# Kernel optimization log

Measured on AMD Instinct MI355X. Metric: run time of the kernel, lower is better.

The kernel has to match this reference:

```python
import jax, jax.numpy as jnp
import numpy as np

B, L, HEADS, D_HEAD = 2, 2048, 16, 64
D_MODEL = HEADS * D_HEAD            # 1024
D_BI = D_MODEL * 4 // 2             # 2048 (bilinear GLU width)
D_PROJ = D_MODEL * 3 + 2 * D_BI
DEPTH = 0                           # block depth < 2 -> token shift active
NEG_INF = -1e10


def _ln(x, g, b, eps=1e-5):
    m = jnp.mean(x, axis=-1, keepdims=True)
    v = jnp.var(x, axis=-1, keepdims=True)
    return (x - m) * jax.lax.rsqrt(v + eps) * g + b


def _shift(x, n):
    # F.pad(x, (0,0,n,-n)): shift along seq dim by n, zero-fill at front
    return jnp.pad(x, ((0, 0), (n, 0), (0, 0)))[:, : x.shape[1], :]


def setup_inputs() -> dict:
    key = jax.random.key(0)
    ks = jax.random.split(key, 3)
    x = jax.random.normal(ks[0], (B, L, D_MODEL), jnp.float32)
    w_in = jax.random.normal(ks[1], (D_MODEL, D_PROJ), jnp.float32) * (D_MODEL ** -0.5)
    # note: torch init zeros out_proj; we use small random weights so backward is non-trivial
    w_out = jax.random.normal(ks[2], (D_MODEL + D_BI, D_MODEL), jnp.float32) * 0.02
    slopes = jnp.concatenate([2.0 ** jnp.linspace(0.0, -6.0, HEADS // 2),
                              jnp.zeros(HEADS - HEADS // 2)]).astype(jnp.float32)
    return {
        "x": x,
        "in_ln_g": jnp.ones(D_MODEL, jnp.float32), "in_ln_b": jnp.zeros(D_MODEL, jnp.float32),
        "mid_ln_g": jnp.ones(D_PROJ, jnp.float32), "mid_ln_b": jnp.zeros(D_PROJ, jnp.float32),
        "out_ln_g": jnp.ones(D_MODEL, jnp.float32), "out_ln_b": jnp.zeros(D_MODEL, jnp.float32),
        "w_in": w_in, "w_out": w_out, "slopes": slopes,
    }


def reference(x, in_ln_g, in_ln_b, mid_ln_g, mid_ln_b, out_ln_g, out_ln_b, w_in, w_out, slopes):
    b, l, d = x.shape
    x = _ln(x, in_ln_g, in_ln_b)
    if DEPTH < 2:
        x = jnp.concatenate([
            _shift(x[..., : d // 4], 1),
            x[..., d // 4: d - d // 8],
            _shift(x[..., d - d // 8:], 2),
        ], axis=-1)
    h = _ln(x @ w_in, mid_ln_g, mid_ln_b)
    q, k, v, p1, p2 = jnp.split(h, [D_MODEL, 2 * D_MODEL, 3 * D_MODEL, 3 * D_MODEL + D_BI], axis=-1)
    to_heads = lambda t: t.reshape(b, l, HEADS, D_HEAD).transpose(0, 2, 1, 3)  # b h l d
    q, k, v = to_heads(q), to_heads(k), to_heads(v)
    logits = jnp.einsum('bhid,bhjd->bhij', q, k) * (D_HEAD ** -0.5)
    pos = jnp.arange(l)
    alibi = pos[None, None, None, :].astype(logits.dtype) * slopes[None, :, None, None]
    causal = jnp.where(pos[:, None] >= pos[None, :], 0.0, NEG_INF).astype(logits.dtype)
    a = jax.nn.softmax(logits + alibi + causal, axis=-1)
    o = jnp.einsum('bhij,bhjd->bhid', a, v).transpose(0, 2, 1, 3).reshape(b, l, d)
    return _ln(jnp.concatenate([o, p1 * p2], axis=-1) @ w_out, out_ln_g, out_ln_b)
```

## Files before the change

### kernel.cpp

```cpp
#include <hip/hip_runtime.h>

#define B_ 2
#define L_ 2048
#define HEADS_ 16
#define DH_ 64
#define DM_ 1024
#define DBI_ 2048
#define DPROJ_ 7168
#define NTOK (B_*L_)
#define DCAT (DM_ + DBI_)

typedef __bf16 bf16;
typedef __attribute__((ext_vector_type(8))) __bf16 bf16x8;
typedef __attribute__((ext_vector_type(4))) float floatx4;

typedef __attribute__((address_space(1))) const void gptr_t;
typedef __attribute__((address_space(3))) void lptr_t;

__device__ __forceinline__ void g2l16(const void* g, void* l) {
    __builtin_amdgcn_global_load_lds((gptr_t*)g, (lptr_t*)l, 16, 0, 0);
}

__global__ __launch_bounds__(256) void transpose_both(const float* __restrict__ w_in,
                                                      const float* __restrict__ w_out,
                                                      bf16* __restrict__ w_inT,
                                                      bf16* __restrict__ w_outT) {
    __shared__ float tile[32][33];
    int l = blockIdx.x;
    const float* in; bf16* outp; int R, C, bx, by;
    if (l < 7168) { in = w_in;  outp = w_inT;  R = DM_;  C = DPROJ_; bx = l % 224; by = l / 224; }
    else { l -= 7168; in = w_out; outp = w_outT; R = DCAT; C = DM_;   bx = l % 32;  by = l / 32; }
    int c0 = bx * 32, r0 = by * 32;
    int x = threadIdx.x & 31, y = threadIdx.x >> 5;
    for (int i = 0; i < 32; i += 8)
        tile[y + i][x] = in[(size_t)(r0 + y + i) * C + (c0 + x)];
    __syncthreads();
    for (int i = 0; i < 32; i += 8)
        outp[(size_t)(c0 + y + i) * R + (r0 + x)] = (bf16)tile[x][y + i];
}

__global__ __launch_bounds__(256) void ln_shift(const float* __restrict__ x,
                                                const float* __restrict__ g,
                                                const float* __restrict__ bb,
                                                bf16* __restrict__ xs) {
    int tok = blockIdx.x;
    int b = tok / L_, l = tok % L_;
    const float* row = x + (size_t)tok * DM_;
    float vals[4];
    float s = 0.f, s2 = 0.f;
    for (int i = 0; i < 4; i++) {
        float v = row[threadIdx.x + i * 256];
        vals[i] = v; s += v; s2 += v * v;
    }
    __shared__ float red[2][4];
    for (int o = 32; o; o >>= 1) { s += __shfl_xor(s, o); s2 += __shfl_xor(s2, o); }
    int w = threadIdx.x >> 6;
    if ((threadIdx.x & 63) == 0) { red[0][w] = s; red[1][w] = s2; }
    __syncthreads();
    s  = red[0][0] + red[0][1] + red[0][2] + red[0][3];
    s2 = red[1][0] + red[1][1] + red[1][2] + red[1][3];
    float mean = s * (1.f / DM_);
    float var  = s2 * (1.f / DM_) - mean * mean;
    float rstd = rsqrtf(var + 1e-5f);
    for (int i = 0; i < 4; i++) {
        int c = threadIdx.x + i * 256;
        float y = (vals[i] - mean) * rstd * g[c] + bb[c];
        int shift = (c < 256) ? 1 : ((c >= 896) ? 2 : 0);
        int dl = l + shift;
        if (dl < L_) xs[((size_t)b * L_ + dl) * DM_ + c] = (bf16)y;
        if (l == 0 && shift) {
            xs[((size_t)b * L_ + 0) * DM_ + c] = (bf16)0.f;
            if (shift == 2) xs[((size_t)b * L_ + 1) * DM_ + c] = (bf16)0.f;
        }
    }
}

__global__ __launch_bounds__(256, 2) void gemm1_k(const bf16* __restrict__ A,
                                                  const bf16* __restrict__ Bt,
                                                  bf16* __restrict__ C) {
    const int K = DM_, N = DPROJ_;
    int lin = blockIdx.x;
    int chunk = lin >> 7, within = lin & 127;
    int m0 = (within >> 3) * 256;
    int n0 = (chunk * 8 + (within & 7)) * 128;
    __shared__ bf16 As[2][256 * 32];
    __shared__ bf16 Bs[2][128 * 32];
    int t = threadIdx.x, lane = t & 63, wave = t >> 6;
    int c = lane & 15, quad = lane >> 4;
    int wm = wave * 64;
    auto stage = [&](int k0, int bsel) {
        #pragma unroll
        for (int s = 0; s < 4; s++) {
            int f = s * 256 + t;
            int row = f >> 2, kp = (f & 3) * 8;
            g2l16(A + (size_t)(m0 + row) * K + k0 + kp, &As[bsel][f * 8]);
        }
        #pragma unroll
        for (int s = 0; s < 2; s++) {
            int f = s * 256 + t;
            int row = f >> 2, kp = (f & 3) * 8;
            g2l16(Bt + (size_t)(n0 + row) * K + k0 + kp, &Bs[bsel][f * 8]);
        }
    };
    floatx4 acc[4][8] = {};
    stage(0, 0);
    int buf = 0;
    for (int k0 = 0; k0 < K; k0 += 32) {
        __syncthreads();
        if (k0 + 32 < K) stage(k0 + 32, buf ^ 1);
        bf16x8 af[4], bfr[8];
        #pragma unroll
        for (int i = 0; i < 4; i++)
            af[i] = *(const bf16x8*)&As[buf][(wm + i * 16 + c) * 32 + quad * 8];
        #pragma unroll
        for (int j = 0; j < 8; j++)
            bfr[j] = *(const bf16x8*)&Bs[buf][(j * 16 + c) * 32 + quad * 8];
        #pragma unroll
        for (int i = 0; i < 4; i++)
            #pragma unroll
            for (int j = 0; j < 8; j++)
                acc[i][j] = __builtin_amdgcn_mfma_f32_16x16x32_bf16(af[i], bfr[j], acc[i][j], 0, 0, 0);
        buf ^= 1;
    }
    #pragma unroll
    for (int i = 0; i < 4; i++)
        #pragma unroll
        for (int j = 0; j < 8; j++)
            #pragma unroll
            for (int r = 0; r < 4; r++) {
                int row = m0 + wm + i * 16 + quad * 4 + r;
                int col = n0 + j * 16 + c;
                C[(size_t)row * N + col] = (bf16)acc[i][j][r];
            }
}

__global__ __launch_bounds__(256) void gemm2_sk(const bf16* __restrict__ A,
                                                const bf16* __restrict__ Bt,
                                                float* __restrict__ P) {
    const int ldA = DCAT, N = DM_;
    int m0 = blockIdx.x * 128, n0 = blockIdx.y * 128, kz = blockIdx.z;
    const bf16* Ak = A + kz * 1024;
    const bf16* Btk = Bt + kz * 1024;
    float* C = P + (size_t)kz * NTOK * DM_;
    __shared__ bf16 As[2][128 * 32];
    __shared__ bf16 Bs[2][128 * 32];
    int t = threadIdx.x, lane = t & 63, wave = t >> 6;
    int c = lane & 15, quad = lane >> 4;
    int wm = (wave >> 1) * 64, wn = (wave & 1) * 64;
    auto stage = [&](int k0, int bsel) {
        #pragma unroll
        for (int s = 0; s < 2; s++) {
            int f = s * 256 + t;
            int row = f >> 2, kp = (f & 3) * 8;
            g2l16(Ak + (size_t)(m0 + row) * ldA + k0 + kp, &As[bsel][f * 8]);
            g2l16(Btk + (size_t)(n0 + row) * ldA + k0 + kp, &Bs[bsel][f * 8]);
        }
    };
    floatx4 acc[4][4] = {};
    stage(0, 0);
    int buf = 0;
    for (int k0 = 0; k0 < 1024; k0 += 32) {
        __syncthreads();
        if (k0 + 32 < 1024) stage(k0 + 32, buf ^ 1);
        bf16x8 af[4], bfr[4];
        #pragma unroll
        for (int i = 0; i < 4; i++)
            af[i] = *(const bf16x8*)&As[buf][(wm + i * 16 + c) * 32 + quad * 8];
        #pragma unroll
        for (int j = 0; j < 4; j++)
            bfr[j] = *(const bf16x8*)&Bs[buf][(wn + j * 16 + c) * 32 + quad * 8];
        #pragma unroll
        for (int i = 0; i < 4; i++)
            #pragma unroll
            for (int j = 0; j < 4; j++)
                acc[i][j] = __builtin_amdgcn_mfma_f32_16x16x32_bf16(af[i], bfr[j], acc[i][j], 0, 0, 0);
        buf ^= 1;
    }
    #pragma unroll
    for (int i = 0; i < 4; i++)
        #pragma unroll
        for (int j = 0; j < 4; j++)
            #pragma unroll
            for (int r = 0; r < 4; r++) {
                int row = m0 + wm + i * 16 + quad * 4 + r;
                int col = n0 + wn + j * 16 + c;
                C[(size_t)row * N + col] = acc[i][j][r];
            }
}

__global__ __launch_bounds__(256) void mid_ln_fused(const bf16* __restrict__ h,
                                                    const float* __restrict__ g,
                                                    const float* __restrict__ bb,
                                                    bf16* __restrict__ Qp,
                                                    bf16* __restrict__ Kp,
                                                    bf16* __restrict__ Vn,
                                                    bf16* __restrict__ A2) {
    int tok = blockIdx.x;
    int b = tok >> 11, l = tok & 2047;
    size_t base = (size_t)tok * DPROJ_;
    int t = threadIdx.x;
    float v[28];
    float s = 0.f, s2 = 0.f;
    for (int i = 0; i < 28; i++) {
        v[i] = (float)h[base + t + i * 256];
        s += v[i]; s2 += v[i] * v[i];
    }
    __shared__ float red[2][4];
    for (int o = 32; o; o >>= 1) { s += __shfl_xor(s, o); s2 += __shfl_xor(s2, o); }
    int w = t >> 6;
    if ((t & 63) == 0) { red[0][w] = s; red[1][w] = s2; }
    __syncthreads();
    s  = red[0][0] + red[0][1] + red[0][2] + red[0][3];
    s2 = red[1][0] + red[1][1] + red[1][2] + red[1][3];
    float mean = s * (1.f / DPROJ_);
    float var  = s2 * (1.f / DPROJ_) - mean * mean;
    float rstd = rsqrtf(var + 1e-5f);
    #pragma unroll
    for (int i = 0; i < 28; i++) {
        int c = t + i * 256;
        v[i] = (v[i] - mean) * rstd * g[c] + bb[c];
    }
    #pragma unroll
    for (int i = 0; i < 12; i++) {
        int c = t + i * 256;
        int sec = c >> 10;
        int cc = c & 1023;
        int hh = cc >> 6, d = cc & 63;
        size_t idx = (((size_t)b * HEADS_ + hh) * L_ + l) * DH_ + d;
        bf16* dst = (sec == 0) ? Qp : (sec == 1) ? Kp : Vn;
        dst[idx] = (bf16)v[i];
    }
    #pragma unroll
    for (int i = 12; i < 20; i++) {
        int c = t + i * 256;
        A2[(size_t)tok * DCAT + DM_ + (c - 3 * DM_)] = (bf16)(v[i] * v[i + 8]);
    }
}

__global__ __launch_bounds__(256) void vt_pack(const bf16* __restrict__ Vn,
                                               bf16* __restrict__ Vt) {
    __shared__ bf16 tile[32][33];
    int bh = blockIdx.z;
    const bf16* in = Vn + (size_t)bh * L_ * DH_;
    bf16* out = Vt + (size_t)bh * DH_ * L_;
    int l0 = blockIdx.x * 32, d0 = blockIdx.y * 32;
    int x = threadIdx.x & 31, y = threadIdx.x >> 5;
    for (int i = 0; i < 32; i += 8)
        tile[y + i][x] = in[(size_t)(l0 + y + i) * DH_ + d0 + x];
    __syncthreads();
    for (int i = 0; i < 32; i += 8)
        out[(size_t)(d0 + y + i) * L_ + l0 + x] = tile[x][y + i];
}

__global__ __launch_bounds__(256, 4) void attn4(const bf16* __restrict__ Qp,
                                                const bf16* __restrict__ Kp,
                                                const bf16* __restrict__ Vt,
                                                const float* __restrict__ slopes,
                                                bf16* __restrict__ A2) {
    int hd = blockIdx.y, b = blockIdx.z;
    int lin = blockIdx.x + 32 * blockIdx.y + 512 * blockIdx.z;
    int xr = blockIdx.x;
    int qt = ((lin >> 8) & 1) ? (31 - xr) : xr;
    int q0 = qt * 64;
    int t = threadIdx.x, lane = t & 63, wave = t >> 6;
    int quad = lane >> 4, c = lane & 15;
    __shared__ bf16 Ks[2 * 64 * 32];
    __shared__ bf16 Vs[2 * 64 * 32];
    __shared__ bf16 Ps[4][16 * 72];
    int bh = b * HEADS_ + hd;
    const bf16* Qb = Qp + (size_t)bh * L_ * DH_;
    const bf16* Kb = Kp + (size_t)bh * L_ * DH_;
    const bf16* Vb = Vt + (size_t)bh * DH_ * L_;
    const float LOG2E = 1.44269504f;
    float slopeL2 = slopes[hd] * LOG2E;
    const float qscale = 0.125f * LOG2E;

    bf16x8 qf[2];
    int qrow = q0 + wave * 16 + c;
    qf[0] = *(const bf16x8*)(Qb + (size_t)qrow * DH_ + quad * 8);
    qf[1] = *(const bf16x8*)(Qb + (size_t)qrow * DH_ + 32 + quad * 8);
    floatx4 accO[4] = {};
    float lsum[4];
    float mrow[4];
    int i_row0 = q0 + wave * 16 + quad * 4;
    #pragma unroll
    for (int r = 0; r < 4; r++) {
        lsum[r] = 0.f;
        mrow[r] = slopeL2 * (float)(i_row0 + r) + 20.0f;
    }

    int row = t >> 2, kp = (t & 3) * 8;
    bf16* pw = &Ps[wave][0];
    bf16* pwr = pw + (quad * 4) * 72 + c;
    for (int j0 = 0; j0 <= q0; j0 += 64) {
        #pragma unroll
        for (int s = 0; s < 2; s++) {
            g2l16(Kb + (size_t)(j0 + row) * DH_ + s * 32 + kp, &Ks[(s * 256 + t) * 8]);
            g2l16(Vb + (size_t)row * L_ + j0 + s * 32 + kp, &Vs[(s * 256 + t) * 8]);
        }
        __syncthreads();

        bool diag = (j0 == q0);
        #pragma unroll
        for (int nt = 0; nt < 4; nt++) {
            floatx4 sacc = {};
            bf16x8 kf0 = *(const bf16x8*)&Ks[(nt * 16 + c) * 32 + quad * 8];
            bf16x8 kf1 = *(const bf16x8*)&Ks[2048 + (nt * 16 + c) * 32 + quad * 8];
            sacc = __builtin_amdgcn_mfma_f32_16x16x32_bf16(qf[0], kf0, sacc, 0, 0, 0);
            sacc = __builtin_amdgcn_mfma_f32_16x16x32_bf16(qf[1], kf1, sacc, 0, 0, 0);
            int j = j0 + nt * 16 + c;
            float aj = slopeL2 * (float)j;
            #pragma unroll
            for (int r = 0; r < 4; r++) {
                float p = exp2f(fmaf(sacc[r], qscale, aj) - mrow[r]);
                if (diag) p = (j <= i_row0 + r) ? p : 0.f;
                lsum[r] += p;
                pwr[r * 72 + nt * 16] = (bf16)p;
            }
        }
        bf16x8 pf0 = *(const bf16x8*)&pw[c * 72 + quad * 8];
        bf16x8 pf1 = *(const bf16x8*)&pw[c * 72 + 32 + quad * 8];
        #pragma unroll
        for (int nt = 0; nt < 4; nt++) {
            bf16x8 vf0 = *(const bf16x8*)&Vs[(nt * 16 + c) * 32 + quad * 8];
            bf16x8 vf1 = *(const bf16x8*)&Vs[2048 + (nt * 16 + c) * 32 + quad * 8];
            accO[nt] = __builtin_amdgcn_mfma_f32_16x16x32_bf16(pf0, vf0, accO[nt], 0, 0, 0);
            accO[nt] = __builtin_amdgcn_mfma_f32_16x16x32_bf16(pf1, vf1, accO[nt], 0, 0, 0);
        }
        __syncthreads();
    }
    #pragma unroll
    for (int r = 0; r < 4; r++) {
        float l = lsum[r];
        l += __shfl_xor(l, 1);
        l += __shfl_xor(l, 2);
        l += __shfl_xor(l, 4);
        l += __shfl_xor(l, 8);
        lsum[r] = 1.f / l;
    }
    #pragma unroll
    for (int r = 0; r < 4; r++) {
        size_t orow = (size_t)b * L_ + q0 + wave * 16 + quad * 4 + r;
        #pragma unroll
        for (int nt = 0; nt < 4; nt++)
            A2[orow * DCAT + hd * DH_ + nt * 16 + c] = (bf16)(accO[nt][r] * lsum[r]);
    }
}

__global__ __launch_bounds__(256) void out_ln3(const float* __restrict__ P,
                                               const float* __restrict__ g,
                                               const float* __restrict__ bb,
                                               float* __restrict__ out) {
    size_t base = (size_t)blockIdx.x * DM_;
    const size_t stride = (size_t)NTOK * DM_;
    float v[4];
    float s = 0.f, s2 = 0.f;
    for (int i = 0; i < 4; i++) {
        size_t idx = base + threadIdx.x + i * 256;
        v[i] = P[idx] + P[idx + stride] + P[idx + 2 * stride];
        s += v[i]; s2 += v[i] * v[i];
    }
    __shared__ float red[2][4];
    for (int o = 32; o; o >>= 1) { s += __shfl_xor(s, o); s2 += __shfl_xor(s2, o); }
    int w = threadIdx.x >> 6;
    if ((threadIdx.x & 63) == 0) { red[0][w] = s; red[1][w] = s2; }
    __syncthreads();
    s  = red[0][0] + red[0][1] + red[0][2] + red[0][3];
    s2 = red[1][0] + red[1][1] + red[1][2] + red[1][3];
    float mean = s * (1.f / DM_);
    float var  = s2 * (1.f / DM_) - mean * mean;
    float rstd = rsqrtf(var + 1e-5f);
    for (int i = 0; i < 4; i++) {
        int c = threadIdx.x + i * 256;
        out[base + c] = (v[i] - mean) * rstd * g[c] + bb[c];
    }
}

extern "C" void kernel_launch(void* const* d_in, const int* in_sizes, int n_in,
                              void* d_out, int out_size, void* d_ws, size_t ws_size,
                              hipStream_t stream) {
    const float* x     = (const float*)d_in[0];
    const float* in_g  = (const float*)d_in[1];
    const float* in_b  = (const float*)d_in[2];
    const float* mid_g = (const float*)d_in[3];
    const float* mid_b = (const float*)d_in[4];
    const float* out_g = (const float*)d_in[5];
    const float* out_b = (const float*)d_in[6];
    const float* w_in  = (const float*)d_in[7];
    const float* w_out = (const float*)d_in[8];
    const float* slopes = (const float*)d_in[9];
    float* out = (float*)d_out;

    char* ws = (char*)d_ws;
    size_t off = 0;
    auto alloc = [&](size_t n) { char* p = ws + off; off += (n + 255) & ~(size_t)255; return p; };
    bf16* w_inT  = (bf16*)alloc((size_t)DPROJ_ * DM_ * 2);
    bf16* w_outT = (bf16*)alloc((size_t)DM_ * DCAT * 2);
    bf16* xs     = (bf16*)alloc((size_t)NTOK * DM_ * 2);
    bf16* h      = (bf16*)alloc((size_t)NTOK * DPROJ_ * 2);
    bf16* A2     = (bf16*)alloc((size_t)NTOK * DCAT * 2);
    bf16* Qp     = (bf16*)alloc((size_t)NTOK * DM_ * 2);
    bf16* Kp     = (bf16*)alloc((size_t)NTOK * DM_ * 2);
    bf16* Vn     = (bf16*)alloc((size_t)NTOK * DM_ * 2);
    bf16* Vt = xs;
    float* P = (float*)h;

    hipLaunchKernelGGL(transpose_both, dim3(7168 + 3072), dim3(256), 0, stream,
                       w_in, w_out, w_inT, w_outT);
    hipLaunchKernelGGL(ln_shift, dim3(NTOK), dim3(256), 0, stream, x, in_g, in_b, xs);
    hipLaunchKernelGGL(gemm1_k, dim3(896), dim3(256), 0, stream, xs, w_inT, h);
    hipLaunchKernelGGL(mid_ln_fused, dim3(NTOK), dim3(256), 0, stream, h, mid_g, mid_b,
                       Qp, Kp, Vn, A2);
    hipLaunchKernelGGL(vt_pack, dim3(L_ / 32, DH_ / 32, B_ * HEADS_), dim3(256), 0, stream, Vn, Vt);
    hipLaunchKernelGGL(attn4, dim3(32, HEADS_, B_), dim3(256), 0, stream, Qp, Kp, Vt, slopes, A2);
    hipLaunchKernelGGL(gemm2_sk, dim3(NTOK / 128, DM_ / 128, 3), dim3(256), 0, stream,
                       A2, w_outT, P);
    hipLaunchKernelGGL(out_ln3, dim3(NTOK), dim3(256), 0, stream, P, out_g, out_b, out);
}
```

Measured before the change: 320.4 us.

## Rewrite input-projection GEMM with 256x256 tiles, 8 waves, and swizzled LDS pipeline

The first GEMM moves from 256x128 tiles with 4 waves and K-step 32 to 256x256 tiles with 8 waves and K-step 64. It adds an XOR-swizzled LDS layout to avoid bank conflicts and an XCD-aware block-to-tile mapping. It also adds an interleaved schedule that issues the next tile's global-to-LDS loads between MFMA phases, using explicit barriers, waitcnts and setprio. The aim is more data reuse per LDS load and more hidden memory latency. The cost is 128 KB of LDS per block, which likely limits occupancy to one block per CU, plus fragile hand-tuned synchronisation.

```diff
diff --git a/kernel.cpp b/kernel.cpp
--- a/kernel.cpp
+++ b/kernel.cpp
@@ -75,61 +75,109 @@
     }
 }
 
-__global__ __launch_bounds__(256, 2) void gemm1_k(const bf16* __restrict__ A,
-                                                  const bf16* __restrict__ Bt,
-                                                  bf16* __restrict__ C) {
+__global__ __launch_bounds__(512, 2) void gemm1_8p(const bf16* __restrict__ A,
+                                                   const bf16* __restrict__ Bt,
+                                                   bf16* __restrict__ C) {
     const int K = DM_, N = DPROJ_;
     int lin = blockIdx.x;
-    int chunk = lin >> 7, within = lin & 127;
-    int m0 = (within >> 3) * 256;
-    int n0 = (chunk * 8 + (within & 7)) * 128;
-    __shared__ bf16 As[2][256 * 32];
-    __shared__ bf16 Bs[2][128 * 32];
-    int t = threadIdx.x, lane = t & 63, wave = t >> 6;
+    int xcd = lin & 7, idx = lin >> 3;
+    int mt = (xcd >> 2) * 8 + idx / 7;
+    int nt = (xcd & 3) * 7 + idx % 7;
+    int m0 = mt * 256, n0 = nt * 256;
+
+    __shared__ bf16 As[2][256 * 64];
+    __shared__ bf16 Bs[2][256 * 64];
+
+    int t = threadIdx.x;
+    int lane = t & 63;
     int c = lane & 15, quad = lane >> 4;
-    int wm = wave * 64;
-    auto stage = [&](int k0, int bsel) {
-        #pragma unroll
-        for (int s = 0; s < 4; s++) {
-            int f = s * 256 + t;
-            int row = f >> 2, kp = (f & 3) * 8;
-            g2l16(A + (size_t)(m0 + row) * K + k0 + kp, &As[bsel][f * 8]);
-        }
+    int wave = t >> 6;
+    int wm = (wave >> 2) * 128;
+    int wn = (wave & 3) * 64;
+
+    auto stageA = [&](int k0, int bsel, int h) {
         #pragma unroll
         for (int s = 0; s < 2; s++) {
-            int f = s * 256 + t;
-            int row = f >> 2, kp = (f & 3) * 8;
-            g2l16(Bt + (size_t)(n0 + row) * K + k0 + kp, &Bs[bsel][f * 8]);
+            int g = h * 1024 + s * 512 + t;
+            int row = g >> 3;
+            int kc = (g & 7) ^ (row & 7);
+            g2l16(A + (size_t)(m0 + row) * K + (k0 + kc * 8), &As[bsel][g * 8]);
         }
     };
-    floatx4 acc[4][8] = {};
-    stage(0, 0);
-    int buf = 0;
-    for (int k0 = 0; k0 < K; k0 += 32) {
-        __syncthreads();
-        if (k0 + 32 < K) stage(k0 + 32, buf ^ 1);
-        bf16x8 af[4], bfr[8];
-        #pragma unroll
-        for (int i = 0; i < 4; i++)
-            af[i] = *(const bf16x8*)&As[buf][(wm + i * 16 + c) * 32 + quad * 8];
-        #pragma unroll
-        for (int j = 0; j < 8; j++)
-            bfr[j] = *(const bf16x8*)&Bs[buf][(j * 16 + c) * 32 + quad * 8];
-        #pragma unroll
-        for (int i = 0; i < 4; i++)
-            #pragma unroll
-            for (int j = 0; j < 8; j++)
-                acc[i][j] = __builtin_amdgcn_mfma_f32_16x16x32_bf16(af[i], bfr[j], acc[i][j], 0, 0, 0);
-        buf ^= 1;
-    }
-    #pragma unroll
-    for (int i = 0; i < 4; i++)
-        #pragma unroll
-        for (int j = 0; j < 8; j++)
+    auto stageB = [&](int k0, int bsel, int h) {
+        #pragma unroll
+        for (int s = 0; s < 2; s++) {
+            int g = h * 1024 + s * 512 + t;
+            int row = g >> 3;
+            int kc = (g & 7) ^ (row & 7);
+            g2l16(Bt + (size_t)(n0 + row) * K + (k0 + kc * 8), &Bs[bsel][g * 8]);
+        }
+    };
+
+    floatx4 acc[8][4] = {};
+
+    stageA(0, 0, 0); stageA(0, 0, 1);
+    stageB(0, 0, 0); stageB(0, 0, 1);
+    stageB(64, 1, 0); stageB(64, 1, 1);
+    asm volatile("s_waitcnt vmcnt(4)" ::: "memory");
+    __builtin_amdgcn_s_barrier();
+
+    const int nT = K / 64;
+    for (int tt = 0; tt < nT; ++tt) {
+        int cur = tt & 1, nxt = cur ^ 1;
+        int k1 = (tt + 1) << 6, k2 = (tt + 2) << 6;
+        bool doA = (tt + 1 < nT), doB = (tt + 2 < nT);
+        bf16x8 bfr[4][2];
+        #pragma unroll
+        for (int p = 0; p < 4; p++) {
+            if (p == 0) {
+                #pragma unroll
+                for (int j = 0; j < 4; j++)
+                    #pragma unroll
+                    for (int s = 0; s < 2; s++)
+                        bfr[j][s] = *(const bf16x8*)&Bs[cur][(wn + j * 16 + c) * 64
+                                                            + (((s * 4 + quad) ^ (c & 7)) * 8)];
+            }
+            bf16x8 af[2][2];
+            #pragma unroll
+            for (int ii = 0; ii < 2; ii++)
+                #pragma unroll
+                for (int s = 0; s < 2; s++)
+                    af[ii][s] = *(const bf16x8*)&As[cur][(wm + (p * 2 + ii) * 16 + c) * 64
+                                                         + (((s * 4 + quad) ^ (c & 7)) * 8)];
+            if      (p == 0) { if (doA) stageA(k1, nxt, 0); }
+            else if (p == 1) { if (doA) stageA(k1, nxt, 1); }
+            else if (p == 2) { if (doB) stageB(k2, cur, 0); }
+            else             { if (doB) stageB(k2, cur, 1); }
+            __builtin_amdgcn_s_barrier();
+            asm volatile("s_waitcnt lgkmcnt(0)" ::: "memory");
+            __builtin_amdgcn_sched_barrier(0);
+            __builtin_amdgcn_s_setprio(1);
+            #pragma unroll
+            for (int ii = 0; ii < 2; ii++)
+                #pragma unroll
+                for (int j = 0; j < 4; j++)
+                    #pragma unroll
+                    for (int s = 0; s < 2; s++)
+                        acc[p * 2 + ii][j] = __builtin_amdgcn_mfma_f32_16x16x32_bf16(
+                            af[ii][s], bfr[j][s], acc[p * 2 + ii][j], 0, 0, 0);
+            __builtin_amdgcn_s_setprio(0);
+            if (p == 3) {
+                if (doB) asm volatile("s_waitcnt vmcnt(4)" ::: "memory");
+                else     asm volatile("s_waitcnt vmcnt(0)" ::: "memory");
+            }
+            __builtin_amdgcn_s_barrier();
+        }
+    }
+
+    #pragma unroll
+    for (int i = 0; i < 8; i++)
+        #pragma unroll
+        for (int j = 0; j < 4; j++)
             #pragma unroll
             for (int r = 0; r < 4; r++) {
                 int row = m0 + wm + i * 16 + quad * 4 + r;
-                int col = n0 + j * 16 + c;
+                int col = n0 + wn + j * 16 + c;
                 C[(size_t)row * N + col] = (bf16)acc[i][j][r];
             }
 }
@@ -408,7 +456,7 @@
     hipLaunchKernelGGL(transpose_both, dim3(7168 + 3072), dim3(256), 0, stream,
                        w_in, w_out, w_inT, w_outT);
     hipLaunchKernelGGL(ln_shift, dim3(NTOK), dim3(256), 0, stream, x, in_g, in_b, xs);
-    hipLaunchKernelGGL(gemm1_k, dim3(896), dim3(256), 0, stream, xs, w_inT, h);
+    hipLaunchKernelGGL(gemm1_8p, dim3(448), dim3(512), 0, stream, xs, w_inT, h);
     hipLaunchKernelGGL(mid_ln_fused, dim3(NTOK), dim3(256), 0, stream, h, mid_g, mid_b,
                        Qp, Kp, Vn, A2);
     hipLaunchKernelGGL(vt_pack, dim3(L_ / 32, DH_ / 32, B_ * HEADS_), dim3(256), 0, stream, Vn, Vt);
```

Result: faster. 311.3 us (-2.8%).
